# Optimization experiments

Measured on AMD Instinct MI355X. Metric: run time of the kernel, lower is better.

## Reference

```python
import jax, jax.numpy as jnp
import numpy as np

D_MODEL = 1024
N_HEADS = 16
D_K = D_MODEL // N_HEADS  # 64
SCALE = 1.0 / np.sqrt(D_K).astype(np.float32)


def setup_inputs() -> dict:
    key = jax.random.key(0)
    kx, kq, kk, kv, ko = jax.random.split(key, 5)
    B, S = 2, 2048
    s = 0.02  # keep pre-softmax logits in a sane range
    return {
        "x": jax.random.normal(kx, (B, S, D_MODEL), dtype=jnp.float32),
        "Wq": jax.random.normal(kq, (D_MODEL, D_MODEL), dtype=jnp.float32) * s,
        "Wk": jax.random.normal(kk, (D_MODEL, D_MODEL), dtype=jnp.float32) * s,
        "Wv": jax.random.normal(kv, (D_MODEL, D_MODEL), dtype=jnp.float32) * s,
        "Wo": jax.random.normal(ko, (D_MODEL, D_MODEL), dtype=jnp.float32) * s,
    }


def reference(x, Wq, Wk, Wv, Wo):
    # x: [B, S, D]; nn.Linear(bias=False) computes x @ W.T
    B, S, D = x.shape
    H, dk = N_HEADS, D_K

    def proj(W):
        # [B, S, D] -> [B, H, S, dk]
        return (x @ W.T).reshape(B, S, H, dk).transpose(0, 2, 1, 3)

    q = proj(Wq)
    k = proj(Wk)
    v = proj(Wv)

    # Flash tiling with online softmax is exact full attention (no mask):
    scores = jnp.einsum("bhqd,bhkd->bhqk", q, k) * SCALE  # [B,H,S,S]
    p = jax.nn.softmax(scores, axis=-1)
    o = jnp.einsum("bhqk,bhkd->bhqd", p, v)               # [B,H,S,dk]

    o = o.transpose(0, 2, 1, 3).reshape(B, S, D)
    return o @ Wo.T
```

## Files before the change

### kernel.cpp

```cpp
#include <hip/hip_runtime.h>
#include <cstdint>

typedef __attribute__((ext_vector_type(8))) __bf16 bf16x8;
typedef __attribute__((ext_vector_type(4))) float f32x4;
using u16 = unsigned short;
using u32 = unsigned int;

#define D_MODEL 1024
#define N_HEADS 16
#define D_K     64
#define SEQ     2048
#define BATCH   2
#define NTOKENS (BATCH * SEQ)
#define SCALE   0.125f
#define LOG2E   1.44269504088896340736f
#define C2      (SCALE * LOG2E)

__device__ __forceinline__ u16 f32_to_bf16(float f) {
    union { float f; u32 u; } v; v.f = f;
    u32 r = (v.u + 0x7fffu + ((v.u >> 16) & 1u)) >> 16;
    return (u16)r;
}

__device__ __forceinline__ u32 cvt_pk_bf16(float a, float b) {
    u32 r;
    asm("v_cvt_pk_bf16_f32 %0, %1, %2" : "=v"(r) : "v"(a), "v"(b));
    return r;
}

typedef const __attribute__((address_space(1))) u32* gas_ptr;
typedef __attribute__((address_space(3))) u32* las_ptr;
__device__ __forceinline__ void gl2lds16(const u16* g, u16* l) {
    __builtin_amdgcn_global_load_lds((gas_ptr)g, (las_ptr)l, 16, 0, 0);
}

__global__ __launch_bounds__(256) void cvt_all(const float* __restrict__ x,
                                               const float* __restrict__ Wq, const float* __restrict__ Wk,
                                               const float* __restrict__ Wv, const float* __restrict__ Wo,
                                               u16* __restrict__ xb,
                                               u16* __restrict__ wq, u16* __restrict__ wk,
                                               u16* __restrict__ wv, u16* __restrict__ wo) {
    const int NX = NTOKENS * D_MODEL;
    size_t i = (size_t)(blockIdx.x * 256 + threadIdx.x) * 4;
    const float* src; u16* dst; size_t off;
    if (i < (size_t)NX) { src = x; dst = xb; off = i; }
    else {
        size_t j = i - NX;
        int w = (int)(j >> 20);
        off = j & ((1u << 20) - 1);
        src = (w == 0) ? Wq : (w == 1) ? Wk : (w == 2) ? Wv : Wo;
        dst = (w == 0) ? wq : (w == 1) ? wk : (w == 2) ? wv : wo;
    }
    float4 f = *(const float4*)(src + off);
    u32 lo = (u32)f32_to_bf16(f.x) | ((u32)f32_to_bf16(f.y) << 16);
    u32 hi = (u32)f32_to_bf16(f.z) | ((u32)f32_to_bf16(f.w) << 16);
    uint2 o; o.x = lo; o.y = hi;
    size_t osw = (off & ~(size_t)63) | ((((off >> 3) & 7) ^ ((off >> 10) & 7)) << 3) | (off & 7);
    *(uint2*)(dst + osw) = o;
}

__device__ __forceinline__ void gemm_core_128(const u16* __restrict__ Ab,
                                              const u16* __restrict__ Bb,
                                              u16* __restrict__ sm,
                                              f32x4 acc[4][4]) {
    const int tid  = threadIdx.x;
    const int wave = tid >> 6, lane = tid & 63;
    const int quad = lane >> 4, l4 = lane & 15, s7 = l4 & 7;
    const int wm = wave >> 1, wn = wave & 1;

    const int srow = tid >> 3, sch = tid & 7;
    const u16* Asrc = Ab + (size_t)srow * D_MODEL + sch * 8;
    const u16* Bsrc = Bb + (size_t)srow * D_MODEL + sch * 8;

#define STG8(base_, kt_) do {                                                         \
    const size_t ko_ = (size_t)(kt_) * 64;                                            \
    u16* const Ad_ = sm + (base_) + wave * 512;                                       \
    u16* const Bd_ = sm + (base_) + 8192 + wave * 512;                                \
    _Pragma("unroll")                                                                 \
    for (int c_ = 0; c_ < 4; c_++)                                                    \
        gl2lds16(Asrc + (size_t)c_ * 32 * D_MODEL + ko_, Ad_ + c_ * 2048);            \
    _Pragma("unroll")                                                                 \
    for (int c_ = 0; c_ < 4; c_++)                                                    \
        gl2lds16(Bsrc + (size_t)c_ * 32 * D_MODEL + ko_, Bd_ + c_ * 2048);            \
} while (0)

    STG8(0, 0);
    asm volatile("s_waitcnt vmcnt(0)" ::: "memory");
    __builtin_amdgcn_s_barrier();

    for (int kt = 0; kt < 16; ++kt) {
        const int cur = (kt & 1) << 14;
        if (kt < 15) {
            if (kt & 1) STG8(0, kt + 1); else STG8(16384, kt + 1);
        }
        const u16* Ar = sm + cur;
        const u16* Br = sm + cur + 8192;
        bf16x8 af[4][2], bfr[4][2];
#pragma unroll
        for (int mt = 0; mt < 4; mt++) {
            const int row = wm * 64 + mt * 16 + l4;
#pragma unroll
            for (int kk = 0; kk < 2; kk++)
                af[mt][kk] = *(const bf16x8*)&Ar[row * 64 + (((kk << 2) + quad) ^ s7) * 8];
        }
#pragma unroll
        for (int nt = 0; nt < 4; nt++) {
            const int row = wn * 64 + nt * 16 + l4;
#pragma unroll
            for (int kk = 0; kk < 2; kk++)
                bfr[nt][kk] = *(const bf16x8*)&Br[row * 64 + (((kk << 2) + quad) ^ s7) * 8];
        }
        __builtin_amdgcn_s_setprio(1);
#pragma unroll
        for (int kk = 0; kk < 2; kk++)
#pragma unroll
            for (int mt = 0; mt < 4; mt++)
#pragma unroll
                for (int nt = 0; nt < 4; nt++)
                    acc[mt][nt] = __builtin_amdgcn_mfma_f32_16x16x32_bf16(af[mt][kk], bfr[nt][kk], acc[mt][nt], 0, 0, 0);
        __builtin_amdgcn_s_setprio(0);
        asm volatile("s_waitcnt vmcnt(0)" ::: "memory");
        __builtin_amdgcn_s_barrier();
    }
#undef STG8
}

__global__ __launch_bounds__(256, 2) void gemm_qkv(const u16* __restrict__ xb,
                                                   const u16* __restrict__ wq,
                                                   const u16* __restrict__ wk,
                                                   const u16* __restrict__ wv,
                                                   u16* __restrict__ Qb, u16* __restrict__ Kb,
                                                   u16* __restrict__ Vt) {
    __shared__ __align__(16) u16 sm[32768];
    const int bid = blockIdx.x;
    const u16 *Ab, *Bb;
    int m0, n0, sel;
    if (bid < 512) {
        sel = bid >> 8;
        const int t = bid & 255;
        m0 = (t >> 3) * 128; n0 = (t & 7) * 128;
        Ab = xb + (size_t)m0 * D_MODEL;
        Bb = (sel ? wk : wq) + (size_t)n0 * D_MODEL;
    } else {
        sel = 2;
        const int t = bid - 512;
        m0 = (t >> 5) * 128; n0 = (t & 31) * 128;
        Ab = wv + (size_t)m0 * D_MODEL;
        Bb = xb + (size_t)n0 * D_MODEL;
    }

    f32x4 acc[4][4] = {};
    gemm_core_128(Ab, Bb, sm, acc);

    const int lane = threadIdx.x & 63, quad = lane >> 4, l4 = lane & 15;
    const int wave = threadIdx.x >> 6, wm = wave >> 1, wn = wave & 1;
#pragma unroll
    for (int mt = 0; mt < 4; mt++)
#pragma unroll
        for (int nt = 0; nt < 4; nt++)
#pragma unroll
            for (int r = 0; r < 4; r++) {
                const int mrow = wm * 64 + mt * 16 + quad * 4 + r;
                const int ncol = wn * 64 + nt * 16 + l4;
                const float v = acc[mt][nt][r];
                const int m7 = (quad * 4 + r) & 7;
                if (sel == 0) {
                    Qb[(size_t)(m0 + mrow) * D_MODEL + n0 + ncol] = f32_to_bf16(v * C2);
                } else if (sel == 1) {
                    const int csw = (wn * 64) | ((((nt * 2 + (l4 >> 3)) ^ m7) << 3)) | (l4 & 7);
                    Kb[(size_t)(m0 + mrow) * D_MODEL + n0 + csw] = f32_to_bf16(v);
                } else {
                    const int k  = nt * 16 + l4;
                    const int g  = (k >> 2) & 3, c = (k >> 4) & 1, r_ = k & 3;
                    const int s  = (k & 32) | (g * 8 + c * 4 + r_);
                    const int csw = (wn * 64) | ((((s >> 3) ^ m7) << 3)) | (s & 7);
                    Vt[(size_t)(m0 + mrow) * NTOKENS + n0 + csw] = f32_to_bf16(v);
                }
            }
}

__global__ __launch_bounds__(256, 2) void gemm_out(const u16* __restrict__ A,
                                                   const u16* __restrict__ Bw,
                                                   float* __restrict__ C) {
    __shared__ __align__(16) u16 sm[32768];
    const int bid = blockIdx.x;
    const int m0 = (bid >> 3) * 128, n0 = (bid & 7) * 128;

    f32x4 acc[4][4] = {};
    gemm_core_128(A + (size_t)m0 * D_MODEL, Bw + (size_t)n0 * D_MODEL, sm, acc);

    const int lane = threadIdx.x & 63, quad = lane >> 4, l4 = lane & 15;
    const int wave = threadIdx.x >> 6, wm = wave >> 1, wn = wave & 1;
#pragma unroll
    for (int mt = 0; mt < 4; mt++)
#pragma unroll
        for (int nt = 0; nt < 4; nt++)
#pragma unroll
            for (int r = 0; r < 4; r++) {
                const int mrow = wm * 64 + mt * 16 + quad * 4 + r;
                const int ncol = wn * 64 + nt * 16 + l4;
                C[(size_t)(m0 + mrow) * D_MODEL + n0 + ncol] = acc[mt][nt][r];
            }
}

__global__ __launch_bounds__(256, 4) void attn(const u16* __restrict__ Q,
                                               const u16* __restrict__ K,
                                               const u16* __restrict__ Vt,
                                               u16* __restrict__ O) {
    __shared__ __align__(16) u16 smem[16384];
    u16* KsB = smem;
    u16* VsB = smem + 8192;

    const int tid  = threadIdx.x;
    const int wave = tid >> 6, lane = tid & 63;
    const int quad = lane >> 4, l4 = lane & 15;
    const int qg = wave;
    const int bid = blockIdx.x;
    const int h  = (bid & 7) | (((bid >> 3) & 1) << 3);
    const int b  = (bid >> 4) & 1;
    const int q0 = (bid >> 5) * 128;
    const size_t headoff = (size_t)b * SEQ * D_MODEL + (size_t)h * D_K;

    const int srow8 = lane >> 3, sch = lane & 7;
    const u16* srcK = K  + headoff + (size_t)(wave * 16 + srow8) * D_MODEL + sch * 8;
    const u16* srcV = Vt + (size_t)(h * 64 + wave * 16 + srow8) * NTOKENS + (size_t)b * SEQ + sch * 8;
    u16* const dK0 = KsB + (wave * 16) * 64;
    u16* const dK1 = KsB + (wave * 16 + 8) * 64;
    u16* const dV0 = VsB + (wave * 16) * 64;
    u16* const dV1 = VsB + (wave * 16 + 8) * 64;

#define ASTG(buf_, t_) do {                                                  \
    const size_t kt_ = (size_t)(t_) * 64 * D_MODEL;                          \
    const size_t vt_ = (size_t)(t_) * 64;                                    \
    gl2lds16(srcK + kt_,                       dK0 + (buf_));                \
    gl2lds16(srcK + kt_ + 8 * D_MODEL,         dK1 + (buf_));                \
    gl2lds16(srcV + vt_,                       dV0 + (buf_));                \
    gl2lds16(srcV + vt_ + (size_t)8 * NTOKENS, dV1 + (buf_));                \
} while (0)

    bf16x8 qa[2][2];
#pragma unroll
    for (int qs = 0; qs < 2; qs++) {
        const u16* qp = Q + headoff + (size_t)(q0 + qg * 32 + qs * 16 + l4) * D_MODEL + quad * 8;
        qa[qs][0] = *(const bf16x8*)qp;
        qa[qs][1] = *(const bf16x8*)(qp + 32);
    }

    union { u32 u[4]; bf16x8 v; } onesu;
#pragma unroll
    for (int i = 0; i < 4; i++) onesu.u[i] = 0x3F803F80u;

    f32x4 acc_o[2][4] = {};
    f32x4 acc_l[2] = {};
    const int sw7 = l4 & 7;

    ASTG(0, 0);
    asm volatile("s_waitcnt vmcnt(0)" ::: "memory");
    __builtin_amdgcn_s_barrier();

    for (int it = 0; it < 32; ++it) {
        const int cur = (it & 1) ? 4096 : 0;
        if (it < 31) { if (it & 1) ASTG(0, it + 1); else ASTG(4096, it + 1); }
        const u16* ksr = KsB + cur;
        const u16* vsr = VsB + cur;

        union { u32 u[4]; bf16x8 v; } pp[2][2];
#pragma unroll
        for (int kf = 0; kf < 2; kf++) {
            bf16x8 kb[2][2];
#pragma unroll
            for (int n2p = 0; n2p < 2; n2p++) {
                const int krow = kf * 32 + n2p * 16 + l4;
                kb[n2p][0] = *(const bf16x8*)&ksr[krow * 64 + ((quad       ^ sw7) * 8)];
                kb[n2p][1] = *(const bf16x8*)&ksr[krow * 64 + (((4 + quad) ^ sw7) * 8)];
            }
            f32x4 sacc[2][2] = {};
            __builtin_amdgcn_s_setprio(1);
#pragma unroll
            for (int qs = 0; qs < 2; qs++)
#pragma unroll
                for (int n2p = 0; n2p < 2; n2p++) {
                    sacc[qs][n2p] = __builtin_amdgcn_mfma_f32_16x16x32_bf16(kb[n2p][0], qa[qs][0], sacc[qs][n2p], 0, 0, 0);
                    sacc[qs][n2p] = __builtin_amdgcn_mfma_f32_16x16x32_bf16(kb[n2p][1], qa[qs][1], sacc[qs][n2p], 0, 0, 0);
                }
            __builtin_amdgcn_s_setprio(0);
#pragma unroll
            for (int qs = 0; qs < 2; qs++)
#pragma unroll
                for (int n2p = 0; n2p < 2; n2p++) {
                    float p0 = __builtin_amdgcn_exp2f(sacc[qs][n2p][0]);
                    float p1 = __builtin_amdgcn_exp2f(sacc[qs][n2p][1]);
                    float p2 = __builtin_amdgcn_exp2f(sacc[qs][n2p][2]);
                    float p3 = __builtin_amdgcn_exp2f(sacc[qs][n2p][3]);
                    pp[qs][kf].u[n2p * 2]     = cvt_pk_bf16(p0, p1);
                    pp[qs][kf].u[n2p * 2 + 1] = cvt_pk_bf16(p2, p3);
                }
        }

        __builtin_amdgcn_s_setprio(1);
#pragma unroll
        for (int dvt = 0; dvt < 4; dvt++) {
            const int vrow = dvt * 16 + l4;
#pragma unroll
            for (int kf = 0; kf < 2; kf++) {
                bf16x8 vfr = *(const bf16x8*)&vsr[vrow * 64 + ((((kf << 2) + quad) ^ sw7) * 8)];
#pragma unroll
                for (int qs = 0; qs < 2; qs++)
                    acc_o[qs][dvt] = __builtin_amdgcn_mfma_f32_16x16x32_bf16(pp[qs][kf].v, vfr, acc_o[qs][dvt], 0, 0, 0);
            }
        }
#pragma unroll
        for (int qs = 0; qs < 2; qs++)
#pragma unroll
            for (int kf = 0; kf < 2; kf++)
                acc_l[qs] = __builtin_amdgcn_mfma_f32_16x16x32_bf16(pp[qs][kf].v, onesu.v, acc_l[qs], 0, 0, 0);
        __builtin_amdgcn_s_setprio(0);

        asm volatile("s_waitcnt vmcnt(0)" ::: "memory");
        __builtin_amdgcn_s_barrier();
    }

#pragma unroll
    for (int qs = 0; qs < 2; qs++)
#pragma unroll
        for (int r = 0; r < 4; r++) {
            const float linv = 1.f / acc_l[qs][r];
            const int qrow = q0 + qg * 32 + qs * 16 + quad * 4 + r;
#pragma unroll
            for (int dvt = 0; dvt < 4; dvt++) {
                const int csw = (((dvt * 2 + (l4 >> 3)) ^ (qrow & 7)) << 3) | (l4 & 7);
                O[headoff + (size_t)qrow * D_MODEL + csw] = f32_to_bf16(acc_o[qs][dvt][r] * linv);
            }
        }
#undef ASTG
}

extern "C" void kernel_launch(void* const* d_in, const int* in_sizes, int n_in,
                              void* d_out, int out_size, void* d_ws, size_t ws_size,
                              hipStream_t stream) {
    const float* x  = (const float*)d_in[0];
    const float* Wq = (const float*)d_in[1];
    const float* Wk = (const float*)d_in[2];
    const float* Wv = (const float*)d_in[3];
    const float* Wo = (const float*)d_in[4];

    const int NW = D_MODEL * D_MODEL;

    char* ws = (char*)d_ws;
    u16* xb = (u16*)ws;
    u16* wq = (u16*)(ws + (8u << 20));
    u16* wk = wq + NW;
    u16* wv = wk + NW;
    u16* wo = wv + NW;
    u16* Qb  = (u16*)(ws + (16u << 20));
    u16* Kb  = (u16*)(ws + (24u << 20));
    u16* Vtb = (u16*)(ws + (32u << 20));

    cvt_all<<<8192, 256, 0, stream>>>(x, Wq, Wk, Wv, Wo, xb, wq, wk, wv, wo);

    gemm_qkv<<<768, 256, 0, stream>>>(xb, wq, wk, wv, Qb, Kb, Vtb);

    attn<<<512, 256, 0, stream>>>(Qb, Kb, Vtb, xb);

    gemm_out<<<256, 256, 0, stream>>>(xb, wo, (float*)d_out);
}
```

Before: 181.5 us.

## Switch LDS XOR swizzle to a 4-row-group even-chunk pattern across all kernels

Replaces the row&7 XOR swizzle with a swizzle keyed on bits 2-3 of the row, shifted to even chunk offsets. This changes the converted weight/x layout, the K and Vt write layouts (K rows permuted, V column permutation simplified) and the O layout so the reads in the GEMM and attention kernels match. The goal is a different LDS bank-conflict profile for 16-byte fragment reads with the 16x16x32 MFMA lane mapping. Every producer and consumer must agree on the new permutation, and the change can add bank conflicts where the old pattern had none.

Result: no change. 178.2 us (-1.8%).

```diff
diff --git a/kernel.cpp b/kernel.cpp
--- a/kernel.cpp
+++ b/kernel.cpp
@@ -33,6 +33,7 @@
 __device__ __forceinline__ void gl2lds16(const u16* g, u16* l) {
     __builtin_amdgcn_global_load_lds((gas_ptr)g, (las_ptr)l, 16, 0, 0);
 }
+
 
 __global__ __launch_bounds__(256) void cvt_all(const float* __restrict__ x,
                                                const float* __restrict__ Wq, const float* __restrict__ Wk,
@@ -55,7 +56,8 @@
     u32 lo = (u32)f32_to_bf16(f.x) | ((u32)f32_to_bf16(f.y) << 16);
     u32 hi = (u32)f32_to_bf16(f.z) | ((u32)f32_to_bf16(f.w) << 16);
     uint2 o; o.x = lo; o.y = hi;
-    size_t osw = (off & ~(size_t)63) | ((((off >> 3) & 7) ^ ((off >> 10) & 7)) << 3) | (off & 7);
+    size_t osw = (off & ~(size_t)63) |
+                 (((((off >> 3) & 7) ^ (((off >> 12) & 3) << 1)) << 3)) | (off & 7);
     *(uint2*)(dst + osw) = o;
 }
 
@@ -65,7 +67,8 @@
                                               f32x4 acc[4][4]) {
     const int tid  = threadIdx.x;
     const int wave = tid >> 6, lane = tid & 63;
-    const int quad = lane >> 4, l4 = lane & 15, s7 = l4 & 7;
+    const int quad = lane >> 4, l4 = lane & 15;
+    const int s2 = ((l4 >> 2) & 3) << 1;
     const int wm = wave >> 1, wn = wave & 1;
 
     const int srow = tid >> 3, sch = tid & 7;
@@ -101,14 +104,14 @@
             const int row = wm * 64 + mt * 16 + l4;
 #pragma unroll
             for (int kk = 0; kk < 2; kk++)
-                af[mt][kk] = *(const bf16x8*)&Ar[row * 64 + (((kk << 2) + quad) ^ s7) * 8];
+                af[mt][kk] = *(const bf16x8*)&Ar[row * 64 + (((kk << 2) + quad) ^ s2) * 8];
         }
 #pragma unroll
         for (int nt = 0; nt < 4; nt++) {
             const int row = wn * 64 + nt * 16 + l4;
 #pragma unroll
             for (int kk = 0; kk < 2; kk++)
-                bfr[nt][kk] = *(const bf16x8*)&Br[row * 64 + (((kk << 2) + quad) ^ s7) * 8];
+                bfr[nt][kk] = *(const bf16x8*)&Br[row * 64 + (((kk << 2) + quad) ^ s2) * 8];
         }
         __builtin_amdgcn_s_setprio(1);
 #pragma unroll
@@ -163,17 +166,18 @@
                 const int mrow = wm * 64 + mt * 16 + quad * 4 + r;
                 const int ncol = wn * 64 + nt * 16 + l4;
                 const float v = acc[mt][nt][r];
-                const int m7 = (quad * 4 + r) & 7;
                 if (sel == 0) {
                     Qb[(size_t)(m0 + mrow) * D_MODEL + n0 + ncol] = f32_to_bf16(v * C2);
                 } else if (sel == 1) {
-                    const int csw = (wn * 64) | ((((nt * 2 + (l4 >> 3)) ^ m7) << 3)) | (l4 & 7);
-                    Kb[(size_t)(m0 + mrow) * D_MODEL + n0 + csw] = f32_to_bf16(v);
+                    const int k5 = mrow & 31;
+                    const int prow = (mrow & 96) | (((k5 >> 2) & 1) << 4) |
+                                     (((k5 >> 3) & 3) << 2) | (k5 & 3);
+                    const int xr = ((prow >> 2) & 3) << 1;
+                    const int csw = (wn * 64) | (((nt * 2 + (l4 >> 3)) ^ xr) << 3) | (l4 & 7);
+                    Kb[(size_t)(m0 + prow) * D_MODEL + n0 + csw] = f32_to_bf16(v);
                 } else {
-                    const int k  = nt * 16 + l4;
-                    const int g  = (k >> 2) & 3, c = (k >> 4) & 1, r_ = k & 3;
-                    const int s  = (k & 32) | (g * 8 + c * 4 + r_);
-                    const int csw = (wn * 64) | ((((s >> 3) ^ m7) << 3)) | (s & 7);
+                    const int xr = ((mrow >> 2) & 3) << 1;
+                    const int csw = (wn * 64) | (((nt * 2 + (l4 >> 3)) ^ xr) << 3) | (l4 & 7);
                     Vt[(size_t)(m0 + mrow) * NTOKENS + n0 + csw] = f32_to_bf16(v);
                 }
             }
@@ -252,7 +256,7 @@
 
     f32x4 acc_o[2][4] = {};
     f32x4 acc_l[2] = {};
-    const int sw7 = l4 & 7;
+    const int sw2 = ((l4 >> 2) & 3) << 1;
 
     ASTG(0, 0);
     asm volatile("s_waitcnt vmcnt(0)" ::: "memory");
@@ -271,8 +275,8 @@
 #pragma unroll
             for (int n2p = 0; n2p < 2; n2p++) {
                 const int krow = kf * 32 + n2p * 16 + l4;
-                kb[n2p][0] = *(const bf16x8*)&ksr[krow * 64 + ((quad       ^ sw7) * 8)];
-                kb[n2p][1] = *(const bf16x8*)&ksr[krow * 64 + (((4 + quad) ^ sw7) * 8)];
+                kb[n2p][0] = *(const bf16x8*)&ksr[krow * 64 + ((quad       ^ sw2) * 8)];
+                kb[n2p][1] = *(const bf16x8*)&ksr[krow * 64 + (((4 + quad) ^ sw2) * 8)];
             }
             f32x4 sacc[2][2] = {};
             __builtin_amdgcn_s_setprio(1);
@@ -303,7 +307,7 @@
             const int vrow = dvt * 16 + l4;
 #pragma unroll
             for (int kf = 0; kf < 2; kf++) {
-                bf16x8 vfr = *(const bf16x8*)&vsr[vrow * 64 + ((((kf << 2) + quad) ^ sw7) * 8)];
+                bf16x8 vfr = *(const bf16x8*)&vsr[vrow * 64 + ((((kf << 2) + quad) ^ sw2) * 8)];
 #pragma unroll
                 for (int qs = 0; qs < 2; qs++)
                     acc_o[qs][dvt] = __builtin_amdgcn_mfma_f32_16x16x32_bf16(pp[qs][kf].v, vfr, acc_o[qs][dvt], 0, 0, 0);
@@ -328,7 +332,7 @@
             const int qrow = q0 + qg * 32 + qs * 16 + quad * 4 + r;
 #pragma unroll
             for (int dvt = 0; dvt < 4; dvt++) {
-                const int csw = (((dvt * 2 + (l4 >> 3)) ^ (qrow & 7)) << 3) | (l4 & 7);
+                const int csw = (((dvt * 2 + (l4 >> 3)) ^ (quad << 1)) << 3) | (l4 & 7);
                 O[headoff + (size_t)qrow * D_MODEL + csw] = f32_to_bf16(acc_o[qs][dvt][r] * linv);
             }
         }
```
